# Kernel tuning notes

Measured on AMD Instinct MI355X. Metric: run time of the kernel, lower is better.

The kernel has to match this reference:

```python
import jax, jax.numpy as jnp
import numpy as np

MAX_SIGMA = 10.0
TRUNCATE = 4.0
R = int(TRUNCATE * MAX_SIGMA + 0.5)  # 40, static max radius (scipy: int(truncate*sigma+0.5))
L = 2 * R + 1                         # 81


def _make_kernels(sigmas):
    # sigmas: [B] -> kernels [B, L], exactly matching scipy._gaussian_kernel1d
    pos = jnp.arange(-R, R + 1, dtype=sigmas.dtype)          # [L]
    r = jnp.floor(TRUNCATE * sigmas + 0.5)                   # per-sample radius
    w = jnp.exp(-0.5 * (pos[None, :] ** 2) / (sigmas[:, None] ** 2))
    w = w * (jnp.abs(pos)[None, :] <= r[:, None])            # scipy truncation
    return w / jnp.sum(w, axis=-1, keepdims=True)


def _reflect_index(n):
    # symmetric ('reflect' in scipy) boundary indices for pad width R, valid even if R > n
    i = jnp.arange(-R, n + R)
    j = jnp.mod(i, 2 * n)
    return jnp.where(j < n, j, 2 * n - 1 - j)


def _conv_last(x, k):
    # correlate along last axis with reflect boundary; x [..., n], k [L]
    n = x.shape[-1]
    xp = x[..., _reflect_index(n)]                            # [..., n+2R]
    flat = xp.reshape(-1, 1, n + 2 * R)
    out = jax.lax.conv_general_dilated(flat, k[None, None, :],
                                       window_strides=(1,), padding='VALID')
    return out.reshape(x.shape)


def _blur_one(xi, k):
    # xi: [C, H, W]; scipy gaussian_filter with scalar sigma blurs every axis
    for ax in range(xi.ndim):
        xi = jnp.moveaxis(_conv_last(jnp.moveaxis(xi, ax, -1), k), -1, ax)
    return xi


def setup_inputs() -> dict:
    key = jax.random.key(0)
    k1, _ = jax.random.split(key)
    B, C, H, W = 64, 3, 512, 512
    x = jax.random.uniform(k1, (B, C, H, W), dtype=jnp.float32)
    blur_sigmas = jnp.asarray(np.geomspace(0.5, MAX_SIGMA, 10), dtype=jnp.float32)
    fwd_steps = jax.random.randint(jax.random.fold_in(key, 1), (B,), 0, 10, dtype=jnp.int32)
    return {"x": x, "blur_sigmas": blur_sigmas, "fwd_steps": fwd_steps}


def reference(x, blur_sigmas, fwd_steps):
    sigmas = blur_sigmas[fwd_steps]          # [B]
    kernels = _make_kernels(sigmas)          # [B, L]
    return jax.vmap(_blur_one)(x, kernels)   # [B, C, H, W]
```

## Files before the change

### kernel.cpp

```cpp
#include <hip/hip_runtime.h>
#include <hip/hip_bf16.h>

#define RMAX 40
#define LK   81
#define HH   512
#define WW   512
#define CC   3
#define BB   64
#define ROWS 2

typedef unsigned short u16;
typedef __attribute__((ext_vector_type(8))) short short8;
typedef __attribute__((ext_vector_type(4))) float f32x4;

__device__ __forceinline__ u16 f2bf(float f) {
    unsigned u = __float_as_uint(f);
    u += 0x7FFFu + ((u >> 16) & 1u);
    return (u16)(u >> 16);
}
__device__ __forceinline__ float bf2f(u16 s) {
    return __uint_as_float(((unsigned)s) << 16);
}

__global__ __launch_bounds__(256) void prep_kernel(
    const float* __restrict__ sigmas10,
    const int*   __restrict__ steps,
    int*   __restrict__ rbuf,
    float* __restrict__ mbuf,
    float* __restrict__ wbuf,
    u16*   __restrict__ atab)
{
    const int b   = blockIdx.x;
    const int tid = threadIdx.x;
    const float sigma = sigmas10[steps[b]];
    int r = (int)floorf(4.0f * sigma + 0.5f);
    if (r > RMAX) r = RMAX;
    const float s2 = sigma * sigma;

    float sum = 0.0f;
    for (int p = -r; p <= r; ++p)
        sum += expf(-0.5f * (float)(p * p) / s2);
    const float inv = 1.0f / sum;

    if (tid < 128) {
        int p = tid - 56;
        float v = 0.0f;
        if (p >= -r && p <= r)
            v = expf(-0.5f * (float)(p * p) / s2) * inv;
        wbuf[b * 128 + tid] = v;
    }

    if (tid == 0) {
        rbuf[b] = r;
        float Mm[9];
        for (int i = 0; i < 9; ++i) Mm[i] = 0.0f;
        for (int p = -r; p <= r; ++p) {
            float wv = expf(-0.5f * (float)(p * p) / s2) * inv;
            for (int c = 0; c < CC; ++c) {
                int i = c + p;
                int j = ((i % 6) + 6) % 6;
                int cc = (j < 3) ? j : 5 - j;
                Mm[c * 3 + cc] += wv;
            }
        }
        for (int c = 0; c < 3; ++c)
            for (int cc = 0; cc < 3; ++cc)
                mbuf[b * 12 + c * 4 + cc] = Mm[c * 3 + cc];
    }

    u16* ab = atab + (size_t)b * 8192;
    int e = tid * 32;
    for (int ee = 0; ee < 32; ++ee, ++e) {
        int j    = e & 7;
        int lane = (e >> 3) & 63;
        int s    = e >> 9;
        int ch   = s >> 2;
        int half = (s >> 1) & 1;
        int prec = s & 1;
        int m = 32 * ch + ((lane >> 4) << 3) + j - (lane & 15) - 16 * half;
        float wfull = 0.0f;
        if (m >= 0 && m <= 2 * r) {
            int p = m - r;
            wfull = expf(-0.5f * (float)(p * p) / s2) * inv;
        }
        u16 hi = f2bf(wfull);
        u16 val = hi;
        if (prec) val = f2bf(wfull - bf2f(hi));
        ab[e] = val;
    }
}

__global__ __launch_bounds__(256) void passB_kernel(
    const float* __restrict__ x,
    const float* __restrict__ wbuf,
    const float* __restrict__ mbuf,
    const int*   __restrict__ rbuf,
    u16* __restrict__ out1)
{
    __shared__ __align__(16) float mixed[CC * ROWS][WW + 2 * RMAX];

    const int b   = blockIdx.y;
    const int h0  = blockIdx.x * ROWS;
    const int tid = threadIdx.x;
    const int r   = __builtin_amdgcn_readfirstlane(rbuf[b]);

    const float M00 = mbuf[b * 12 + 0], M01 = mbuf[b * 12 + 1], M02 = mbuf[b * 12 + 2];
    const float M10 = mbuf[b * 12 + 4], M11 = mbuf[b * 12 + 5], M12 = mbuf[b * 12 + 6];
    const float M20 = mbuf[b * 12 + 8], M21 = mbuf[b * 12 + 9], M22 = mbuf[b * 12 + 10];

    const float* xb = x + (size_t)b * CC * HH * WW + (size_t)h0 * WW;

    {
        const int row   = tid >> 7;
        const int wbase = (tid & 127) << 2;
        const float* px = xb + (size_t)row * WW + wbase;
        f32x4 c0 = __builtin_nontemporal_load((const f32x4*)px);
        f32x4 c1 = __builtin_nontemporal_load((const f32x4*)(px + HH * WW));
        f32x4 c2 = __builtin_nontemporal_load((const f32x4*)(px + 2 * HH * WW));
        f32x4 m0 = M00 * c0 + M01 * c1 + M02 * c2;
        f32x4 m1 = M10 * c0 + M11 * c1 + M12 * c2;
        f32x4 m2 = M20 * c0 + M21 * c1 + M22 * c2;
        *(f32x4*)&mixed[0 * ROWS + row][RMAX + wbase] = m0;
        *(f32x4*)&mixed[1 * ROWS + row][RMAX + wbase] = m1;
        *(f32x4*)&mixed[2 * ROWS + row][RMAX + wbase] = m2;
    }
    if (tid < 2 * 2 * RMAX) {
        const int row = tid & 1;
        const int k   = tid >> 1;
        const int wi  = (k < RMAX) ? k : (WW + k);
        const int lw  = wi - RMAX;
        const int jm  = lw & (2 * WW - 1);
        const int src = (jm < WW) ? jm : (2 * WW - 1 - jm);
        const float* px = xb + (size_t)row * WW + src;
        float a0 = __builtin_nontemporal_load(px);
        float a1 = __builtin_nontemporal_load(px + HH * WW);
        float a2 = __builtin_nontemporal_load(px + 2 * HH * WW);
        mixed[0 * ROWS + row][wi] = M00 * a0 + M01 * a1 + M02 * a2;
        mixed[1 * ROWS + row][wi] = M10 * a0 + M11 * a1 + M12 * a2;
        mixed[2 * ROWS + row][wi] = M20 * a0 + M21 * a1 + M22 * a2;
    }
    __syncthreads();

    const int t0    = (RMAX - r) & ~3;
    const int n4    = ((r + RMAX + 3 - t0) >> 2) + 1;
    const int kbase = (16 + t0) >> 2;
    const f32x4* K4 = (const f32x4*)(wbuf + b * 128);

#pragma unroll
    for (int k = 0; k < 3; ++k) {
        const int task = tid + 256 * k;
        const int g    = task & 127;
        const int rc   = task >> 7;
        const int w0   = g << 2;

        const int dbase = (w0 + t0) >> 2;
        const f32x4* D4 = (const f32x4*)(&mixed[rc][0]);

        f32x4 Wlo = K4[kbase - 1];
        float acc0 = 0.f, acc1 = 0.f, acc2 = 0.f, acc3 = 0.f;

        for (int s = 0; s < n4; ++s) {
            f32x4 Whi = K4[kbase + s];
            f32x4 D   = D4[dbase + s];
            acc0 += Whi.x * D.x; acc1 += Wlo.w * D.x; acc2 += Wlo.z * D.x; acc3 += Wlo.y * D.x;
            acc0 += Whi.y * D.y; acc1 += Whi.x * D.y; acc2 += Wlo.w * D.y; acc3 += Wlo.z * D.y;
            acc0 += Whi.z * D.z; acc1 += Whi.y * D.z; acc2 += Whi.x * D.z; acc3 += Wlo.w * D.z;
            acc0 += Whi.w * D.w; acc1 += Whi.z * D.w; acc2 += Whi.y * D.w; acc3 += Whi.x * D.w;
            Wlo = Whi;
        }

        ushort4 o;
        o.x = f2bf(acc0); o.y = f2bf(acc1); o.z = f2bf(acc2); o.w = f2bf(acc3);
        const int c = rc >> 1, row = rc & 1;
        u16* dst = out1 + ((size_t)b * CC + c) * HH * WW
                 + (size_t)(h0 + row) * WW + w0;
        *(ushort4*)dst = o;
    }
}

__device__ __forceinline__ int refl512(int i) {
    int jm = i & (2 * HH - 1);
    return (jm < HH) ? jm : (2 * HH - 1 - jm);
}

__global__ __launch_bounds__(256) void passC_kernel(
    const u16* __restrict__ in1,
    const u16* __restrict__ atab,
    const int* __restrict__ rbuf,
    float* __restrict__ out)
{
    const int tid  = threadIdx.x;
    const int lane = tid & 63;
    const int bc   = blockIdx.z;
    const int b    = bc / 3;
    const int r    = __builtin_amdgcn_readfirstlane(rbuf[b]);
    const int h0   = blockIdx.y * 32;
    const int w    = blockIdx.x * 64 + (tid >> 6) * 16 + (lane & 15);
    const int nch  = (2 * r + 63) >> 5;
    const int rowbase = h0 - r + ((lane >> 4) << 3);

    const u16* src = in1 + (size_t)bc * HH * WW + w;
    const short8* at = (const short8*)(atab + (size_t)b * 8192);

    f32x4 acc0 = {0.f, 0.f, 0.f, 0.f};
    f32x4 acc1 = {0.f, 0.f, 0.f, 0.f};

    for (int ch = 0; ch < nch; ++ch) {
        short8 bv;
#pragma unroll
        for (int j = 0; j < 8; ++j) {
            int row = refl512(rowbase + 32 * ch + j);
            bv[j] = (short)src[(size_t)row * WW];
        }
        short8 ah0 = at[(ch * 4 + 0) * 64 + lane];
        short8 al0 = at[(ch * 4 + 1) * 64 + lane];
        short8 ah1 = at[(ch * 4 + 2) * 64 + lane];
        short8 al1 = at[(ch * 4 + 3) * 64 + lane];

        acc0 = __builtin_amdgcn_mfma_f32_16x16x32_bf16(ah0, bv, acc0, 0, 0, 0);
        acc0 = __builtin_amdgcn_mfma_f32_16x16x32_bf16(al0, bv, acc0, 0, 0, 0);
        acc1 = __builtin_amdgcn_mfma_f32_16x16x32_bf16(ah1, bv, acc1, 0, 0, 0);
        acc1 = __builtin_amdgcn_mfma_f32_16x16x32_bf16(al1, bv, acc1, 0, 0, 0);
    }

    const int orow = h0 + ((lane >> 4) << 2);
    float* dst = out + (size_t)bc * HH * WW + (size_t)orow * WW + w;
#pragma unroll
    for (int q = 0; q < 4; ++q) {
        __builtin_nontemporal_store(acc0[q], dst + (size_t)q * WW);
        __builtin_nontemporal_store(acc1[q], dst + (size_t)(q + 16) * WW);
    }
}

extern "C" void kernel_launch(void* const* d_in, const int* in_sizes, int n_in,
                              void* d_out, int out_size, void* d_ws, size_t ws_size,
                              hipStream_t stream)
{
    const float* x      = (const float*)d_in[0];
    const float* sigmas = (const float*)d_in[1];
    const int*   steps  = (const int*)d_in[2];
    float*       out    = (float*)d_out;

    int*   rbuf  = (int*)d_ws;
    float* mbuf  = (float*)((char*)d_ws + 256);
    float* wbuf  = (float*)((char*)d_ws + 4096);
    u16*   atab  = (u16*)((char*)d_ws + 65536);
    u16*   inter = (u16*)((char*)d_ws + 65536 + (1 << 20));

    prep_kernel<<<64, 256, 0, stream>>>(sigmas, steps, rbuf, mbuf, wbuf, atab);

    dim3 gB(HH / ROWS, BB);
    passB_kernel<<<gB, 256, 0, stream>>>(x, wbuf, mbuf, rbuf, inter);

    dim3 gC(WW / 64, HH / 32, BB * CC);
    passC_kernel<<<gC, 256, 0, stream>>>(inter, atab, rbuf, out);
}
```

Before: 409.3 us.

## Use fp16 packed dot2 for width-axis blur with fp16 LDS staging

The width pass now stages the channel-mixed rows in LDS as fp16 rather than fp32. It also precomputes even- and odd-aligned packed fp16 weight pairs so the convolution can use v_dot2 instructions, each thread producing 8 outputs instead of 4. Each block now handles 4 rows instead of 2, which halves the block count and widens stores to 8 bf16 values. The aim is to roughly halve the ALU work and LDS traffic in pass B. The cost is lower intermediate precision: fp16 inputs and weights, though accumulation stays in fp32.

```diff
diff --git a/kernel.cpp b/kernel.cpp
--- a/kernel.cpp
+++ b/kernel.cpp
@@ -2,16 +2,19 @@
 #include <hip/hip_bf16.h>
 
 #define RMAX 40
-#define LK   81
 #define HH   512
 #define WW   512
 #define CC   3
 #define BB   64
-#define ROWS 2
+#define ROWS 4
+#define LROW 592
 
 typedef unsigned short u16;
 typedef __attribute__((ext_vector_type(8))) short short8;
 typedef __attribute__((ext_vector_type(4))) float f32x4;
+typedef _Float16 h2 __attribute__((ext_vector_type(2)));
+typedef _Float16 h8 __attribute__((ext_vector_type(8)));
+typedef __attribute__((ext_vector_type(8))) u16 u16x8;
 
 __device__ __forceinline__ u16 f2bf(float f) {
     unsigned u = __float_as_uint(f);
@@ -21,14 +24,24 @@
 __device__ __forceinline__ float bf2f(u16 s) {
     return __uint_as_float(((unsigned)s) << 16);
 }
+__device__ __forceinline__ u16 h2u16(_Float16 h) { return __builtin_bit_cast(u16, h); }
+
+__device__ __forceinline__ float fdot2w(h2 a, unsigned wpk, float c) {
+#if __has_builtin(__builtin_amdgcn_fdot2)
+    return __builtin_amdgcn_fdot2(a, __builtin_bit_cast(h2, wpk), c, false);
+#else
+    h2 wv = __builtin_bit_cast(h2, wpk);
+    return c + (float)a.x * (float)wv.x + (float)a.y * (float)wv.y;
+#endif
+}
 
 __global__ __launch_bounds__(256) void prep_kernel(
     const float* __restrict__ sigmas10,
     const int*   __restrict__ steps,
-    int*   __restrict__ rbuf,
-    float* __restrict__ mbuf,
-    float* __restrict__ wbuf,
-    u16*   __restrict__ atab)
+    int*      __restrict__ rbuf,
+    float*    __restrict__ mbuf,
+    unsigned* __restrict__ ptab,
+    u16*      __restrict__ atab)
 {
     const int b   = blockIdx.x;
     const int tid = threadIdx.x;
@@ -42,12 +55,23 @@
         sum += expf(-0.5f * (float)(p * p) / s2);
     const float inv = 1.0f / sum;
 
-    if (tid < 128) {
-        int p = tid - 56;
-        float v = 0.0f;
-        if (p >= -r && p <= r)
-            v = expf(-0.5f * (float)(p * p) / s2) * inv;
-        wbuf[b * 128 + tid] = v;
+    auto kval = [&](int i) -> float {
+        int p = i - 56;
+        if (p < -r || p > r) return 0.0f;
+        return expf(-0.5f * (float)(p * p) / s2) * inv;
+    };
+
+    if (tid < 64) {
+        float a = kval(2 * tid), bb = kval(2 * tid + 1);
+        unsigned pk = (unsigned)h2u16((_Float16)a)
+                    | ((unsigned)h2u16((_Float16)bb) << 16);
+        ptab[b * 128 + tid] = pk;
+    } else if (tid < 128) {
+        int m = tid - 64;
+        float a = kval(2 * m - 1), bb = kval(2 * m);
+        unsigned pk = (unsigned)h2u16((_Float16)a)
+                    | ((unsigned)h2u16((_Float16)bb) << 16);
+        ptab[b * 128 + 64 + m] = pk;
     }
 
     if (tid == 0) {
@@ -91,13 +115,13 @@
 }
 
 __global__ __launch_bounds__(256) void passB_kernel(
-    const float* __restrict__ x,
-    const float* __restrict__ wbuf,
-    const float* __restrict__ mbuf,
-    const int*   __restrict__ rbuf,
+    const float*    __restrict__ x,
+    const unsigned* __restrict__ ptab,
+    const float*    __restrict__ mbuf,
+    const int*      __restrict__ rbuf,
     u16* __restrict__ out1)
 {
-    __shared__ __align__(16) float mixed[CC * ROWS][WW + 2 * RMAX];
+    __shared__ __align__(16) u16 mixs[CC * ROWS][LROW];
 
     const int b   = blockIdx.y;
     const int h0  = blockIdx.x * ROWS;
@@ -110,71 +134,91 @@
 
     const float* xb = x + (size_t)b * CC * HH * WW + (size_t)h0 * WW;
 
-    {
-        const int row   = tid >> 7;
-        const int wbase = (tid & 127) << 2;
-        const float* px = xb + (size_t)row * WW + wbase;
+#pragma unroll
+    for (int it = 0; it < 2; ++it) {
+        int idx = tid + 256 * it;
+        int row = idx >> 7;
+        int w   = (idx & 127) << 2;
+        const float* px = xb + (size_t)row * WW + w;
         f32x4 c0 = __builtin_nontemporal_load((const f32x4*)px);
         f32x4 c1 = __builtin_nontemporal_load((const f32x4*)(px + HH * WW));
         f32x4 c2 = __builtin_nontemporal_load((const f32x4*)(px + 2 * HH * WW));
         f32x4 m0 = M00 * c0 + M01 * c1 + M02 * c2;
         f32x4 m1 = M10 * c0 + M11 * c1 + M12 * c2;
         f32x4 m2 = M20 * c0 + M21 * c1 + M22 * c2;
-        *(f32x4*)&mixed[0 * ROWS + row][RMAX + wbase] = m0;
-        *(f32x4*)&mixed[1 * ROWS + row][RMAX + wbase] = m1;
-        *(f32x4*)&mixed[2 * ROWS + row][RMAX + wbase] = m2;
-    }
-    if (tid < 2 * 2 * RMAX) {
-        const int row = tid & 1;
-        const int k   = tid >> 1;
-        const int wi  = (k < RMAX) ? k : (WW + k);
-        const int lw  = wi - RMAX;
-        const int jm  = lw & (2 * WW - 1);
-        const int src = (jm < WW) ? jm : (2 * WW - 1 - jm);
-        const float* px = xb + (size_t)row * WW + src;
-        float a0 = __builtin_nontemporal_load(px);
-        float a1 = __builtin_nontemporal_load(px + HH * WW);
-        float a2 = __builtin_nontemporal_load(px + 2 * HH * WW);
-        mixed[0 * ROWS + row][wi] = M00 * a0 + M01 * a1 + M02 * a2;
-        mixed[1 * ROWS + row][wi] = M10 * a0 + M11 * a1 + M12 * a2;
-        mixed[2 * ROWS + row][wi] = M20 * a0 + M21 * a1 + M22 * a2;
+        ushort4 o0, o1, o2;
+        o0.x = h2u16((_Float16)m0.x); o0.y = h2u16((_Float16)m0.y);
+        o0.z = h2u16((_Float16)m0.z); o0.w = h2u16((_Float16)m0.w);
+        o1.x = h2u16((_Float16)m1.x); o1.y = h2u16((_Float16)m1.y);
+        o1.z = h2u16((_Float16)m1.z); o1.w = h2u16((_Float16)m1.w);
+        o2.x = h2u16((_Float16)m2.x); o2.y = h2u16((_Float16)m2.y);
+        o2.z = h2u16((_Float16)m2.z); o2.w = h2u16((_Float16)m2.w);
+        *(ushort4*)&mixs[0 * ROWS + row][RMAX + w] = o0;
+        *(ushort4*)&mixs[1 * ROWS + row][RMAX + w] = o1;
+        *(ushort4*)&mixs[2 * ROWS + row][RMAX + w] = o2;
+    }
+#pragma unroll
+    for (int it = 0; it < 2; ++it) {
+        int hidx = tid + 256 * it;
+        if (hidx < ROWS * 2 * RMAX) {
+            int row = hidx & 3;
+            int pos = hidx >> 2;
+            int wi  = (pos < RMAX) ? pos : (WW + pos);
+            int lw  = wi - RMAX;
+            int jm  = lw & (2 * WW - 1);
+            int src = (jm < WW) ? jm : (2 * WW - 1 - jm);
+            const float* px = xb + (size_t)row * WW + src;
+            float a0 = __builtin_nontemporal_load(px);
+            float a1 = __builtin_nontemporal_load(px + HH * WW);
+            float a2 = __builtin_nontemporal_load(px + 2 * HH * WW);
+            mixs[0 * ROWS + row][wi] = h2u16((_Float16)(M00 * a0 + M01 * a1 + M02 * a2));
+            mixs[1 * ROWS + row][wi] = h2u16((_Float16)(M10 * a0 + M11 * a1 + M12 * a2));
+            mixs[2 * ROWS + row][wi] = h2u16((_Float16)(M20 * a0 + M21 * a1 + M22 * a2));
+        }
     }
     __syncthreads();
 
-    const int t0    = (RMAX - r) & ~3;
-    const int n4    = ((r + RMAX + 3 - t0) >> 2) + 1;
-    const int kbase = (16 + t0) >> 2;
-    const f32x4* K4 = (const f32x4*)(wbuf + b * 128);
+    const int i0off = (RMAX - r) & ~7;
+    const int base0 = (16 + i0off) >> 1;
+    const int nck   = ((((RMAX - r) & 7) + 7 + 2 * r) >> 3) + 1;
+    const unsigned* et = ptab + b * 128;
+    const unsigned* ot = et + 64;
 
 #pragma unroll
     for (int k = 0; k < 3; ++k) {
         const int task = tid + 256 * k;
-        const int g    = task & 127;
-        const int rc   = task >> 7;
-        const int w0   = g << 2;
-
-        const int dbase = (w0 + t0) >> 2;
-        const f32x4* D4 = (const f32x4*)(&mixed[rc][0]);
-
-        f32x4 Wlo = K4[kbase - 1];
-        float acc0 = 0.f, acc1 = 0.f, acc2 = 0.f, acc3 = 0.f;
-
-        for (int s = 0; s < n4; ++s) {
-            f32x4 Whi = K4[kbase + s];
-            f32x4 D   = D4[dbase + s];
-            acc0 += Whi.x * D.x; acc1 += Wlo.w * D.x; acc2 += Wlo.z * D.x; acc3 += Wlo.y * D.x;
-            acc0 += Whi.y * D.y; acc1 += Whi.x * D.y; acc2 += Wlo.w * D.y; acc3 += Wlo.z * D.y;
-            acc0 += Whi.z * D.z; acc1 += Whi.y * D.z; acc2 += Whi.x * D.z; acc3 += Wlo.w * D.z;
-            acc0 += Whi.w * D.w; acc1 += Whi.z * D.w; acc2 += Whi.y * D.w; acc3 += Whi.x * D.w;
-            Wlo = Whi;
-        }
-
-        ushort4 o;
-        o.x = f2bf(acc0); o.y = f2bf(acc1); o.z = f2bf(acc2); o.w = f2bf(acc3);
-        const int c = rc >> 1, row = rc & 1;
-        u16* dst = out1 + ((size_t)b * CC + c) * HH * WW
+        const int g    = task & 63;
+        const int rc   = task >> 6;
+        const int w0   = g << 3;
+        const u16* L   = &mixs[rc][0];
+        const int ib   = w0 + i0off;
+
+        float a0 = 0.f, a1 = 0.f, a2 = 0.f, a3 = 0.f;
+        float a4 = 0.f, a5 = 0.f, a6 = 0.f, a7 = 0.f;
+
+        for (int c = 0; c < nck; ++c) {
+            h8 D = *(const h8*)(L + ib + 8 * c);
+            int mi = base0 + 4 * c;
+#pragma unroll
+            for (int u = 0; u < 4; ++u) {
+                h2 dp = { D[2 * u], D[2 * u + 1] };
+                a0 = fdot2w(dp, et[mi + u],     a0);
+                a1 = fdot2w(dp, ot[mi + u],     a1);
+                a2 = fdot2w(dp, et[mi + u - 1], a2);
+                a3 = fdot2w(dp, ot[mi + u - 1], a3);
+                a4 = fdot2w(dp, et[mi + u - 2], a4);
+                a5 = fdot2w(dp, ot[mi + u - 2], a5);
+                a6 = fdot2w(dp, et[mi + u - 3], a6);
+                a7 = fdot2w(dp, ot[mi + u - 3], a7);
+            }
+        }
+
+        const int cch = rc >> 2, row = rc & 3;
+        u16x8 o = { f2bf(a0), f2bf(a1), f2bf(a2), f2bf(a3),
+                    f2bf(a4), f2bf(a5), f2bf(a6), f2bf(a7) };
+        u16* dst = out1 + ((size_t)b * CC + cch) * HH * WW
                  + (size_t)(h0 + row) * WW + w0;
-        *(ushort4*)dst = o;
+        *(u16x8*)dst = o;
     }
 }
 
@@ -241,16 +285,16 @@
     const int*   steps  = (const int*)d_in[2];
     float*       out    = (float*)d_out;
 
-    int*   rbuf  = (int*)d_ws;
-    float* mbuf  = (float*)((char*)d_ws + 256);
-    float* wbuf  = (float*)((char*)d_ws + 4096);
-    u16*   atab  = (u16*)((char*)d_ws + 65536);
-    u16*   inter = (u16*)((char*)d_ws + 65536 + (1 << 20));
-
-    prep_kernel<<<64, 256, 0, stream>>>(sigmas, steps, rbuf, mbuf, wbuf, atab);
+    int*      rbuf  = (int*)d_ws;
+    float*    mbuf  = (float*)((char*)d_ws + 256);
+    unsigned* ptab  = (unsigned*)((char*)d_ws + 4096);
+    u16*      atab  = (u16*)((char*)d_ws + 65536);
+    u16*      inter = (u16*)((char*)d_ws + 65536 + (1 << 20));
+
+    prep_kernel<<<64, 256, 0, stream>>>(sigmas, steps, rbuf, mbuf, ptab, atab);
 
     dim3 gB(HH / ROWS, BB);
-    passB_kernel<<<gB, 256, 0, stream>>>(x, wbuf, mbuf, rbuf, inter);
+    passB_kernel<<<gB, 256, 0, stream>>>(x, ptab, mbuf, rbuf, inter);
 
     dim3 gC(WW / 64, HH / 32, BB * CC);
     passC_kernel<<<gC, 256, 0, stream>>>(inter, atab, rbuf, out);
```

Result: no change. 414.7 us (+1.3%).
